# Kernel tuning notes

Hardware: AMD Instinct MI355X
Metric: run time of the kernel (lower is better)

Reference implementation:

```python
import jax, jax.numpy as jnp
import numpy as np


def pool_windows(a, k):
    # a: [..., H, W] with k == stride (non-overlapping windows)
    lead = a.shape[:-2]
    H, W = a.shape[-2], a.shape[-1]
    a = a.reshape(*lead, H // k, k, W // k, k)
    a = jnp.moveaxis(a, -3, -2)            # [..., Ho, Wo, k, k]
    return a.reshape(*lead, H // k, W // k, k * k)


def setup_inputs() -> dict:
    key = jax.random.key(0)
    k1, k2 = jax.random.split(key)
    S, C, H, W = 258, 64, 64, 64
    x = jax.random.normal(k1, (S, C, H, W), dtype=jnp.float32)
    # noise layer (last row) is nonnegative by convention
    x = x.at[-1].set(jnp.abs(x[-1]))
    x_true = jax.random.normal(k2, (C, H, W), dtype=jnp.float32)
    return {"x": x, "x_true": x_true, "kernel_size": 2, "stride": 2}


def reference(x, x_true, kernel_size, stride):
    # Zonotope/interval abstract transformer for MaxPool2d.
    # x: [S, C, H, W]; row 0 = center, rows 1:-1 = eps coeffs, row -1 = noise.
    assert kernel_size == stride
    k = kernel_size

    # Interval bounds per element (sum-of-abs reduction over symbol layers)
    eps_abs = jnp.sum(jnp.abs(x[1:]), axis=0)           # [C, H, W]
    lo = x[0] - eps_abs
    hi = x[0] + eps_abs

    xw = pool_windows(x, k)                              # [S, C, Ho, Wo, K]
    lw = pool_windows(lo, k)                             # [C, Ho, Wo, K]
    uw = pool_windows(hi, k)
    K = xw.shape[-1]

    # Candidate: window element with the largest lower bound
    i_star = jnp.argmax(lw, axis=-1)                     # [C, Ho, Wo]
    l_star = jnp.take_along_axis(lw, i_star[..., None], axis=-1)[..., 0]
    u_max = jnp.max(uw, axis=-1)

    # Max upper bound among the other window elements
    oh = jnp.arange(K) == i_star[..., None]              # one-hot of i_star
    u_other = jnp.max(jnp.where(oh, -jnp.inf, uw), axis=-1)

    # Exact case: the candidate dominates every other element -> pass its
    # affine form through. Otherwise fall back to the sound interval box
    # [l_star, u_max] (center +/- half-width in the noise layer).
    exact = l_star >= u_other                            # [C, Ho, Wo]

    gathered = jnp.take_along_axis(
        xw, i_star[None, ..., None], axis=-1)[..., 0]    # [S, C, Ho, Wo]

    box_center = 0.5 * (l_star + u_max)
    box_noise = 0.5 * (u_max - l_star)

    out_center = jnp.where(exact, gathered[0], box_center)
    out_eps = jnp.where(exact[None], gathered[1:-1], 0.0)
    out_noise = jnp.where(exact, jnp.abs(gathered[-1]), box_noise)

    x_out = jnp.concatenate(
        [out_center[None], out_eps, out_noise[None]], axis=0)

    out_abs = jnp.sum(jnp.abs(x_out[1:]), axis=0)
    x_min = x_out[0] - out_abs
    x_max = x_out[0] + out_abs

    x_true_out = jnp.max(pool_windows(x_true, k), axis=-1)
    return x_out, x_min, x_max, x_true_out
```

## Files before the change

### kernel.cpp

```cpp
#include <hip/hip_runtime.h>
#include <math.h>

#define S   258
#define C   64
#define H   64
#define W   64
#define HO  32
#define WO  32
#define NP  (C * HO * WO)
#define L   (C * H * W)
#define NCHUNK 8

__global__ __launch_bounds__(256) void k_partial(const float* __restrict__ x,
                                                 float* __restrict__ part) {
    const int p     = blockIdx.x * 256 + threadIdx.x;
    const int chunk = blockIdx.y;
    const int c  = p >> 10;
    const int hw = p & 1023;
    const int ho = hw >> 5;
    const int wo = hw & 31;
    const int base = c * (H * W) + (ho * 2) * W + wo * 2;

    const int s0 = 1 + (257 * chunk) / NCHUNK;
    const int s1 = 1 + (257 * (chunk + 1)) / NCHUNK;

    float a0 = 0.f, a1 = 0.f, a2 = 0.f, a3 = 0.f;
    const float* px = x + (size_t)s0 * L + base;
    for (int s = s0; s < s1; ++s) {
        float2 r0 = *(const float2*)(px);
        float2 r1 = *(const float2*)(px + W);
        a0 += fabsf(r0.x); a1 += fabsf(r0.y);
        a2 += fabsf(r1.x); a3 += fabsf(r1.y);
        px += L;
    }
    float* q = part + (size_t)chunk * (4 * NP) + p;
    q[0]        = a0;
    q[NP]       = a1;
    q[2 * NP]   = a2;
    q[3 * NP]   = a3;
}

__global__ __launch_bounds__(256) void k_meta(const float* __restrict__ x,
                                              const float* __restrict__ x_true,
                                              const float* __restrict__ part,
                                              float* __restrict__ mcenter,
                                              float* __restrict__ mnoise,
                                              int*   __restrict__ mpos,
                                              float* __restrict__ out_tail) {
    const int p = blockIdx.x * 256 + threadIdx.x;

    float e0 = 0.f, e1 = 0.f, e2 = 0.f, e3 = 0.f;
    #pragma unroll
    for (int j = 0; j < NCHUNK; ++j) {
        const float* q = part + (size_t)j * (4 * NP) + p;
        e0 += q[0];
        e1 += q[NP];
        e2 += q[2 * NP];
        e3 += q[3 * NP];
    }

    const int c  = p >> 10;
    const int hw = p & 1023;
    const int ho = hw >> 5;
    const int wo = hw & 31;
    const int base = c * (H * W) + (ho * 2) * W + wo * 2;

    float2 r0 = *(const float2*)(x + base);
    float2 r1 = *(const float2*)(x + base + W);
    float x0[4]  = { r0.x, r0.y, r1.x, r1.y };
    float eps[4] = { e0, e1, e2, e3 };
    float lo[4], hi[4];
    #pragma unroll
    for (int e = 0; e < 4; ++e) { lo[e] = x0[e] - eps[e]; hi[e] = x0[e] + eps[e]; }

    int istar = 0;
    #pragma unroll
    for (int e = 1; e < 4; ++e) if (lo[e] > lo[istar]) istar = e;

    const float lstar = lo[istar];
    const float umax  = fmaxf(fmaxf(hi[0], hi[1]), fmaxf(hi[2], hi[3]));
    float uoth = -INFINITY;
    #pragma unroll
    for (int e = 0; e < 4; ++e) if (e != istar) uoth = fmaxf(uoth, hi[e]);

    const bool exact = (lstar >= uoth);
    const int  off   = (istar & 1) + (istar >> 1) * W;
    const int  pos   = base + off;

    float center, noise, xmax;
    if (exact) {
        center = x0[istar];
        noise  = fabsf(x[(size_t)(S - 1) * L + pos]);
        xmax   = hi[istar];
    } else {
        center = 0.5f * (lstar + umax);
        noise  = 0.5f * (umax - lstar);
        xmax   = umax;
    }

    mcenter[p] = center;
    mnoise[p]  = noise;
    mpos[p]    = exact ? pos : -1;

    out_tail[p]      = lstar;
    out_tail[NP + p] = xmax;

    float2 t0 = *(const float2*)(x_true + base);
    float2 t1 = *(const float2*)(x_true + base + W);
    out_tail[2 * NP + p] = fmaxf(fmaxf(t0.x, t0.y), fmaxf(t1.x, t1.y));
}

__global__ __launch_bounds__(256) void k_write(const float* __restrict__ x,
                                               const float* __restrict__ mcenter,
                                               const float* __restrict__ mnoise,
                                               const int*   __restrict__ mpos,
                                               float* __restrict__ out) {
    const int idx = blockIdx.x * 256 + threadIdx.x;
    const int s = idx >> 16;
    const int p = idx & 65535;
    float v;
    if (s == 0) {
        v = mcenter[p];
    } else if (s == S - 1) {
        v = mnoise[p];
    } else {
        const int pos = mpos[p];
        v = 0.0f;
        if (pos >= 0) v = x[(size_t)s * L + pos];
    }
    out[idx] = v;
}

extern "C" void kernel_launch(void* const* d_in, const int* in_sizes, int n_in,
                              void* d_out, int out_size, void* d_ws, size_t ws_size,
                              hipStream_t stream) {
    const float* x      = (const float*)d_in[0];
    const float* x_true = (const float*)d_in[1];
    float* out = (float*)d_out;

    float* part    = (float*)d_ws;
    float* mcenter = part + (size_t)NCHUNK * 4 * NP;
    float* mnoise  = mcenter + NP;
    int*   mpos    = (int*)(mnoise + NP);

    const int XOUT = S * NP;

    k_partial<<<dim3(NP / 256, NCHUNK), 256, 0, stream>>>(x, part);
    k_meta<<<NP / 256, 256, 0, stream>>>(x, x_true, part, mcenter, mnoise, mpos,
                                         out + XOUT);
    k_write<<<XOUT / 256, 256, 0, stream>>>(x, mcenter, mnoise, mpos, out);
}
```

Before: 401.8 us.

## Fuse reduction and metadata per block; memset output and sparsely gather exact windows

Merges the partial abs-sum reduction and the per-window metadata kernel into one kernel. Each block handles one (c, ho) row pair, sums over symbol layers in 16 groups with float4 loads, and reduces in shared memory. The dense eps-layer write kernel is replaced by a memset of the output plus a gather kernel. That kernel copies coefficients only for windows flagged exact, using an atomic-appended list. This removes the global partial-sum scratch round trip and the per-element gather over the whole output. The cost is an atomic counter and a gather whose speed depends on how many windows are exact.

```diff
diff --git a/kernel.cpp b/kernel.cpp
--- a/kernel.cpp
+++ b/kernel.cpp
@@ -1,134 +1,123 @@
 #include <hip/hip_runtime.h>
 #include <math.h>
 
-#define S   258
-#define C   64
-#define H   64
-#define W   64
-#define HO  32
-#define WO  32
-#define NP  (C * HO * WO)
-#define L   (C * H * W)
-#define NCHUNK 8
+#define S    258
+#define C    64
+#define H    64
+#define W    64
+#define HO   32
+#define WO   32
+#define NP   (C * HO * WO)
+#define L    (C * H * W)
+#define XOUT (S * NP)
 
-__global__ __launch_bounds__(256) void k_partial(const float* __restrict__ x,
-                                                 float* __restrict__ part) {
-    const int p     = blockIdx.x * 256 + threadIdx.x;
-    const int chunk = blockIdx.y;
-    const int c  = p >> 10;
-    const int hw = p & 1023;
-    const int ho = hw >> 5;
-    const int wo = hw & 31;
-    const int base = c * (H * W) + (ho * 2) * W + wo * 2;
+__global__ __launch_bounds__(256) void k_main(const float* __restrict__ x,
+                                              const float* __restrict__ x_true,
+                                              float* __restrict__ out,
+                                              int* __restrict__ counter,
+                                              int2* __restrict__ exlist) {
+    __shared__ float red[16][8][16];
+    __shared__ float eps2[8][16];
 
-    const int s0 = 1 + (257 * chunk) / NCHUNK;
-    const int s1 = 1 + (257 * (chunk + 1)) / NCHUNK;
+    const int b   = blockIdx.x;
+    const int c   = b >> 5;
+    const int ho  = b & 31;
+    const int tid = threadIdx.x;
+    const int sg  = tid >> 4;
+    const int wp  = tid & 15;
 
-    float a0 = 0.f, a1 = 0.f, a2 = 0.f, a3 = 0.f;
-    const float* px = x + (size_t)s0 * L + base;
+    const int rowbase = c * (H * W) + ho * 2 * W;
+    const int A = rowbase + wp * 4;
+
+    const int s0 = 1 + ((257 * sg) >> 4);
+    const int s1 = 1 + ((257 * (sg + 1)) >> 4);
+
+    float a0=0.f,a1=0.f,a2=0.f,a3=0.f,a4=0.f,a5=0.f,a6=0.f,a7=0.f;
+    const float* px = x + (size_t)s0 * L + A;
     for (int s = s0; s < s1; ++s) {
-        float2 r0 = *(const float2*)(px);
-        float2 r1 = *(const float2*)(px + W);
-        a0 += fabsf(r0.x); a1 += fabsf(r0.y);
-        a2 += fabsf(r1.x); a3 += fabsf(r1.y);
+        float4 t = *(const float4*)(px);
+        float4 u = *(const float4*)(px + W);
+        a0 += fabsf(t.x); a1 += fabsf(t.y); a2 += fabsf(t.z); a3 += fabsf(t.w);
+        a4 += fabsf(u.x); a5 += fabsf(u.y); a6 += fabsf(u.z); a7 += fabsf(u.w);
         px += L;
     }
-    float* q = part + (size_t)chunk * (4 * NP) + p;
-    q[0]        = a0;
-    q[NP]       = a1;
-    q[2 * NP]   = a2;
-    q[3 * NP]   = a3;
+    red[sg][0][wp]=a0; red[sg][1][wp]=a1; red[sg][2][wp]=a2; red[sg][3][wp]=a3;
+    red[sg][4][wp]=a4; red[sg][5][wp]=a5; red[sg][6][wp]=a6; red[sg][7][wp]=a7;
+    __syncthreads();
+
+    if (tid < 128) {
+        const int e = tid >> 4, w = tid & 15;
+        float sum = 0.f;
+        #pragma unroll
+        for (int j = 0; j < 16; ++j) sum += red[j][e][w];
+        eps2[e][w] = sum;
+    }
+    __syncthreads();
+
+    if (tid < 32) {
+        const int wo  = tid;
+        const int wq  = wo >> 1;
+        const int odd = wo & 1;
+        float eps[4];
+        eps[0] = eps2[odd * 2 + 0][wq];
+        eps[1] = eps2[odd * 2 + 1][wq];
+        eps[2] = eps2[4 + odd * 2 + 0][wq];
+        eps[3] = eps2[4 + odd * 2 + 1][wq];
+
+        const int wbase = rowbase + wo * 2;
+        float2 r0 = *(const float2*)(x + wbase);
+        float2 r1 = *(const float2*)(x + wbase + W);
+        float x0[4] = { r0.x, r0.y, r1.x, r1.y };
+        float lo[4], hi[4];
+        #pragma unroll
+        for (int e = 0; e < 4; ++e) { lo[e] = x0[e] - eps[e]; hi[e] = x0[e] + eps[e]; }
+
+        int istar = 0;
+        #pragma unroll
+        for (int e = 1; e < 4; ++e) if (lo[e] > lo[istar]) istar = e;
+
+        const float lstar = lo[istar];
+        const float umax  = fmaxf(fmaxf(hi[0], hi[1]), fmaxf(hi[2], hi[3]));
+        float uoth = -INFINITY;
+        #pragma unroll
+        for (int e = 0; e < 4; ++e) if (e != istar) uoth = fmaxf(uoth, hi[e]);
+
+        const bool exact = (lstar >= uoth);
+        const int  pos   = wbase + (istar & 1) + (istar >> 1) * W;
+
+        float center, noise;
+        if (exact) {
+            center = x0[istar];
+            noise  = fabsf(x[(size_t)(S - 1) * L + pos]);
+            int i  = atomicAdd(counter, 1);
+            exlist[i] = make_int2(c * 1024 + ho * 32 + wo, pos);
+        } else {
+            center = 0.5f * (lstar + umax);
+            noise  = 0.5f * (umax - lstar);
+        }
+
+        const int p = c * 1024 + ho * 32 + wo;
+        out[p] = center;
+        out[(size_t)(S - 1) * NP + p] = noise;
+        out[XOUT + p] = lstar;
+        out[XOUT + NP + p] = umax;
+
+        float2 t0 = *(const float2*)(x_true + wbase);
+        float2 t1 = *(const float2*)(x_true + wbase + W);
+        out[XOUT + 2 * NP + p] = fmaxf(fmaxf(t0.x, t0.y), fmaxf(t1.x, t1.y));
+    }
 }
 
-__global__ __launch_bounds__(256) void k_meta(const float* __restrict__ x,
-                                              const float* __restrict__ x_true,
-                                              const float* __restrict__ part,
-                                              float* __restrict__ mcenter,
-                                              float* __restrict__ mnoise,
-                                              int*   __restrict__ mpos,
-                                              float* __restrict__ out_tail) {
-    const int p = blockIdx.x * 256 + threadIdx.x;
-
-    float e0 = 0.f, e1 = 0.f, e2 = 0.f, e3 = 0.f;
-    #pragma unroll
-    for (int j = 0; j < NCHUNK; ++j) {
-        const float* q = part + (size_t)j * (4 * NP) + p;
-        e0 += q[0];
-        e1 += q[NP];
-        e2 += q[2 * NP];
-        e3 += q[3 * NP];
+__global__ __launch_bounds__(256) void k_gather(const float* __restrict__ x,
+                                                const int* __restrict__ counter,
+                                                const int2* __restrict__ exlist,
+                                                float* __restrict__ out) {
+    const int n = counter[0];
+    const int s = 1 + threadIdx.x;
+    for (int i = blockIdx.x; i < n; i += gridDim.x) {
+        const int2 e = exlist[i];
+        out[(size_t)s * NP + e.x] = x[(size_t)s * L + e.y];
     }
-
-    const int c  = p >> 10;
-    const int hw = p & 1023;
-    const int ho = hw >> 5;
-    const int wo = hw & 31;
-    const int base = c * (H * W) + (ho * 2) * W + wo * 2;
-
-    float2 r0 = *(const float2*)(x + base);
-    float2 r1 = *(const float2*)(x + base + W);
-    float x0[4]  = { r0.x, r0.y, r1.x, r1.y };
-    float eps[4] = { e0, e1, e2, e3 };
-    float lo[4], hi[4];
-    #pragma unroll
-    for (int e = 0; e < 4; ++e) { lo[e] = x0[e] - eps[e]; hi[e] = x0[e] + eps[e]; }
-
-    int istar = 0;
-    #pragma unroll
-    for (int e = 1; e < 4; ++e) if (lo[e] > lo[istar]) istar = e;
-
-    const float lstar = lo[istar];
-    const float umax  = fmaxf(fmaxf(hi[0], hi[1]), fmaxf(hi[2], hi[3]));
-    float uoth = -INFINITY;
-    #pragma unroll
-    for (int e = 0; e < 4; ++e) if (e != istar) uoth = fmaxf(uoth, hi[e]);
-
-    const bool exact = (lstar >= uoth);
-    const int  off   = (istar & 1) + (istar >> 1) * W;
-    const int  pos   = base + off;
-
-    float center, noise, xmax;
-    if (exact) {
-        center = x0[istar];
-        noise  = fabsf(x[(size_t)(S - 1) * L + pos]);
-        xmax   = hi[istar];
-    } else {
-        center = 0.5f * (lstar + umax);
-        noise  = 0.5f * (umax - lstar);
-        xmax   = umax;
-    }
-
-    mcenter[p] = center;
-    mnoise[p]  = noise;
-    mpos[p]    = exact ? pos : -1;
-
-    out_tail[p]      = lstar;
-    out_tail[NP + p] = xmax;
-
-    float2 t0 = *(const float2*)(x_true + base);
-    float2 t1 = *(const float2*)(x_true + base + W);
-    out_tail[2 * NP + p] = fmaxf(fmaxf(t0.x, t0.y), fmaxf(t1.x, t1.y));
-}
-
-__global__ __launch_bounds__(256) void k_write(const float* __restrict__ x,
-                                               const float* __restrict__ mcenter,
-                                               const float* __restrict__ mnoise,
-                                               const int*   __restrict__ mpos,
-                                               float* __restrict__ out) {
-    const int idx = blockIdx.x * 256 + threadIdx.x;
-    const int s = idx >> 16;
-    const int p = idx & 65535;
-    float v;
-    if (s == 0) {
-        v = mcenter[p];
-    } else if (s == S - 1) {
-        v = mnoise[p];
-    } else {
-        const int pos = mpos[p];
-        v = 0.0f;
-        if (pos >= 0) v = x[(size_t)s * L + pos];
-    }
-    out[idx] = v;
 }
 
 extern "C" void kernel_launch(void* const* d_in, const int* in_sizes, int n_in,
@@ -138,15 +127,12 @@
     const float* x_true = (const float*)d_in[1];
     float* out = (float*)d_out;
 
-    float* part    = (float*)d_ws;
-    float* mcenter = part + (size_t)NCHUNK * 4 * NP;
-    float* mnoise  = mcenter + NP;
-    int*   mpos    = (int*)(mnoise + NP);
+    int*  counter = (int*)d_ws;
+    int2* exlist  = (int2*)((char*)d_ws + 256);
 
-    const int XOUT = S * NP;
+    hipMemsetAsync(out, 0, (size_t)XOUT * sizeof(float), stream);
+    hipMemsetAsync(counter, 0, sizeof(int), stream);
 
-    k_partial<<<dim3(NP / 256, NCHUNK), 256, 0, stream>>>(x, part);
-    k_meta<<<NP / 256, 256, 0, stream>>>(x, x_true, part, mcenter, mnoise, mpos,
-                                         out + XOUT);
-    k_write<<<XOUT / 256, 256, 0, stream>>>(x, mcenter, mnoise, mpos, out);
+    k_main<<<C * HO, 256, 0, stream>>>(x, x_true, out, counter, exlist);
+    k_gather<<<64, 256, 0, stream>>>(x, counter, exlist, out);
 }
```

Result: faster. 393.7 us (-2.0%).
